# Kernel optimization log

Hardware: AMD Instinct MI355X
Metric: run time of the kernel (lower is better)

## Reference

```python
import jax, jax.numpy as jnp
import numpy as np

# --- static config (matches init_kwargs) ---
T, V, D, H = 4096, 32000, 1024, 16
DH = D // H                      # rope/head dim = 64
E, CAP, K, HOPS = 8, 1024, 2, 3  # non-identity experts, capacity, top-k, hops
MLP = 4 * D
ROPE_BASE = 10000.0
ATTN_IDX = np.array([0, 2, 4, 6])  # experts built with i%2==0 -> Attention
FFN_IDX = np.array([1, 3, 5, 7])   # i%2==1 -> FeedForward
EPS = 1e-6


def rope_cos_sin(t, dh, base):
    inv = 1.0 / (base ** (jnp.arange(0, dh, 2, dtype=jnp.float32) / dh))
    ang = jnp.arange(t, dtype=jnp.float32)[:, None] * inv[None, :]  # [T, dh/2]
    ang = jnp.concatenate([ang, ang], axis=-1)                      # [T, dh]
    return jnp.cos(ang), jnp.sin(ang)


def rotate_half(x):
    h = x.shape[-1] // 2
    return jnp.concatenate([-x[..., h:], x[..., :h]], axis=-1)


def topk_mask(logits, k):
    # boolean [T, E_total] mask of per-row top-k
    _, idx = jax.lax.top_k(logits, k)
    hard = jax.nn.one_hot(idx, logits.shape[-1]).sum(axis=-2)
    return hard.astype(bool)


def capacity_select(mask_te, gate_te, capacity):
    # mask_te: [T,E] bool, gate_te: [T,E] float -> slot [E,C,T], kept [E,T]
    m = mask_te.T                                   # [E, T]
    g = jnp.where(m, gate_te.T, -jnp.inf)           # [E, T]
    cap = int(min(capacity, g.shape[1]))
    _, top_idx = jax.lax.top_k(g, cap)              # [E, C]
    Ee, C = top_idx.shape
    slot = jnp.zeros((Ee, C, g.shape[1]), g.dtype)
    slot = slot.at[jnp.arange(Ee)[:, None], jnp.arange(C)[None, :], top_idx].set(1.0)
    slot = slot * m[:, None, :]                     # drop -inf fill slots
    kept = slot.sum(1).astype(bool)                 # [E, T]
    return slot, kept


def rms_norm(x, w):
    return x * jax.lax.rsqrt(jnp.mean(x * x, axis=-1, keepdims=True) + EPS) * w


def attention_group(x, cos_r, sin_r, wq, wk, wv, wo):
    # x: [G,C,D]; cos_r/sin_r: [G,C,DH]; weights: [G,D,D]
    G, C, _ = x.shape
    q = jnp.einsum('gcd,gde->gce', x, wq).reshape(G, C, H, DH)
    k = jnp.einsum('gcd,gde->gce', x, wk).reshape(G, C, H, DH)
    v = jnp.einsum('gcd,gde->gce', x, wv).reshape(G, C, H, DH)
    c = cos_r[:, :, None, :]
    s = sin_r[:, :, None, :]
    q = q * c + rotate_half(q) * s
    k = k * c + rotate_half(k) * s
    scores = jnp.einsum('gqhd,gkhd->ghqk', q, k) / np.sqrt(DH).astype(np.float32)
    attn = jax.nn.softmax(scores, axis=-1)
    out = jnp.einsum('ghqk,gkhd->gqhd', attn, v).reshape(G, C, D)
    return jnp.einsum('gcd,gde->gce', out, wo)


def ffn_group(x, w1, w2):
    # x: [G,C,D]; w1: [G,D,MLP]; w2: [G,MLP,D]
    return jnp.einsum('gcf,gfd->gcd', jax.nn.gelu(jnp.einsum('gcd,gdf->gcf', x, w1)), w2)


def dna_forward(ids, embed_w, router_w, wq, wk, wv, wo, w1, w2, ln_w):
    h = embed_w[ids]                                     # [T, D]
    cos, sin = rope_cos_sin(T, DH, ROPE_BASE)            # [T, DH]
    for hop in range(HOPS):
        logits = h @ router_w[hop].T                     # [T, E+1]
        probs = jax.nn.softmax(logits, axis=-1)
        mask_full = topk_mask(logits, K)                 # [T, E+1]
        probs_tr = probs[:, :-1]                         # [T, E]
        mask_tr = mask_full[:, :-1]
        slot, kept = capacity_select(mask_tr, probs_tr, CAP)  # [E,C,T], [E,T]
        # dispatch
        xin = jnp.einsum('ect,td->ecd', slot, h)          # [E, C, D]
        cos_r = jnp.einsum('ect,td->ecd', slot, cos)      # [E, C, DH]
        sin_r = jnp.einsum('ect,td->ecd', slot, sin)
        # grouped expert execution (stacked params, vectorized over group dim)
        attn_out = attention_group(xin[ATTN_IDX], cos_r[ATTN_IDX], sin_r[ATTN_IDX],
                                   wq, wk, wv, wo)        # [4, C, D]
        ffn_out = ffn_group(xin[FFN_IDX], w1, w2)         # [4, C, D]
        expert_out = jnp.zeros((E, CAP, D), h.dtype)
        expert_out = expert_out.at[ATTN_IDX].set(attn_out).at[FFN_IDX].set(ffn_out)
        # combine
        combine_w = jnp.where(kept.T, probs_tr, 0.0)      # [T, E]
        rho = combine_w.sum(axis=1, keepdims=True)        # [T, 1]
        combine = jnp.einsum('ecd,ect,et->td', expert_out, slot, combine_w.T)
        h = h + combine - rho * h
    return rms_norm(h, ln_w)


def setup_inputs() -> dict:
    key = jax.random.key(0)
    ks = jax.random.split(key, 10)
    sc = 0.02
    return {
        'ids': jax.random.randint(ks[0], (T,), 0, V),
        'embed_w': jax.random.normal(ks[1], (V, D), jnp.float32) * sc,
        'router_w': jax.random.normal(ks[2], (HOPS, E + 1, D), jnp.float32) * sc,
        'wq': jax.random.normal(ks[3], (4, D, D), jnp.float32) * sc,
        'wk': jax.random.normal(ks[4], (4, D, D), jnp.float32) * sc,
        'wv': jax.random.normal(ks[5], (4, D, D), jnp.float32) * sc,
        'wo': jax.random.normal(ks[6], (4, D, D), jnp.float32) * sc,
        'w1': jax.random.normal(ks[7], (4, D, MLP), jnp.float32) * sc,
        'w2': jax.random.normal(ks[8], (4, MLP, D), jnp.float32) * sc,
        'ln_w': jnp.ones((D,), jnp.float32),
    }


def reference(ids, embed_w, router_w, wq, wk, wv, wo, w1, w2, ln_w):
    return dna_forward(ids, embed_w, router_w, wq, wk, wv, wo, w1, w2, ln_w)
```

## Files before the change

kernel.cpp:

```cpp
#include <hip/hip_runtime.h>
#include <math.h>

#define T_ 4096
#define D_ 1024
#define H_ 16
#define DH_ 64
#define E_ 8
#define CAP_ 1024
#define MLP_ 4096
#define HOPS_ 3

__global__ __launch_bounds__(256) void embed_kernel(
    const int* __restrict__ ids, const float* __restrict__ ew, float* __restrict__ h)
{
  const int t = blockIdx.x;
  const int id = ids[t];
  const int c = threadIdx.x * 4;
  *(float4*)(h + (size_t)t * D_ + c) = *(const float4*)(ew + (size_t)id * D_ + c);
}

__global__ __launch_bounds__(64) void router_kernel(
    const float* __restrict__ h, const float* __restrict__ rw,
    float* __restrict__ probs, float* __restrict__ gmask)
{
  const int t = blockIdx.x;
  const int lane = threadIdx.x;
  __shared__ float hs[D_];
  #pragma unroll
  for (int j = 0; j < 4; ++j)
    *(float4*)&hs[lane * 4 + j * 256] = *(const float4*)(h + (size_t)t * D_ + lane * 4 + j * 256);
  __syncthreads();
  float l9[9];
  #pragma unroll
  for (int e = 0; e < 9; ++e) {
    float s = 0.0f;
    for (int i = lane; i < D_; i += 64) s += hs[i] * rw[e * D_ + i];
    #pragma unroll
    for (int off = 32; off > 0; off >>= 1) s += __shfl_down(s, off);
    l9[e] = s;
  }
  if (lane == 0) {
    float m = l9[0];
    #pragma unroll
    for (int e = 1; e < 9; ++e) m = fmaxf(m, l9[e]);
    float sum = 0.0f;
    float ex[9];
    #pragma unroll
    for (int e = 0; e < 9; ++e) { ex[e] = expf(l9[e] - m); sum += ex[e]; }
    const float inv = 1.0f / sum;
    int b1 = 0;
    #pragma unroll
    for (int e = 1; e < 9; ++e) if (l9[e] > l9[b1]) b1 = e;
    int b2 = (b1 == 0) ? 1 : 0;
    #pragma unroll
    for (int e = 0; e < 9; ++e) if (e != b1 && e != b2 && l9[e] > l9[b2]) b2 = e;
    #pragma unroll
    for (int e = 0; e < 8; ++e) {
      const float pe = ex[e] * inv;
      probs[t * 8 + e] = pe;
      gmask[(size_t)e * T_ + t] = (e == b1 || e == b2) ? pe : -1e30f;
    }
  }
}

__global__ __launch_bounds__(256) void zero_kernel(float* __restrict__ rho, int* __restrict__ cnt)
{
  const int i = blockIdx.x * 256 + threadIdx.x;
  if (i < T_) rho[i] = 0.0f;
  if (i < E_) cnt[i] = 0;
}

__global__ __launch_bounds__(256) void zeroeo_kernel(float* __restrict__ eo)
{
  const size_t i = ((size_t)blockIdx.x * 256 + threadIdx.x) * 4;
  float4 z; z.x = z.y = z.z = z.w = 0.0f;
  *(float4*)(eo + i) = z;
}

__global__ __launch_bounds__(256) void select_kernel(
    const float* __restrict__ gmask, const float* __restrict__ probs,
    int* __restrict__ idx, int* __restrict__ cnt, float* __restrict__ rho)
{
  __shared__ float row[T_];
  const int e = blockIdx.y;
  const int tid = threadIdx.x;
  const float* gr = gmask + (size_t)e * T_;
  #pragma unroll
  for (int j = 0; j < 16; ++j) row[tid + 256 * j] = gr[tid + 256 * j];
  __syncthreads();
  const int t = blockIdx.x * 256 + tid;
  const float g = row[t];
  if (g > -1e29f) {
    int rank = 0;
    for (int tt = 0; tt < T_; ++tt) {
      const float gg = row[tt];
      rank += (gg > g) || (gg == g && tt < t);
    }
    if (rank < CAP_) {
      const int pos = atomicAdd(&cnt[e], 1);
      idx[e * CAP_ + pos] = t;
      atomicAdd(&rho[t], probs[t * 8 + e]);
    }
  }
}

typedef __bf16 bf16x8 __attribute__((ext_vector_type(8)));
typedef float f32x4v __attribute__((ext_vector_type(4)));

union FragU { uint2 u2[2]; bf16x8 v; };

__device__ __forceinline__ unsigned pack_hi2(unsigned u0, unsigned u1)
{
  return (u0 >> 16) | (u1 & 0xFFFF0000u);
}

__device__ __forceinline__ void split8(const float4 a, const float4 b, FragU& h, FragU& l)
{
  const float f[8] = {a.x, a.y, a.z, a.w, b.x, b.y, b.z, b.w};
  unsigned hu[8], lu[8];
  #pragma unroll
  for (int i = 0; i < 8; ++i) {
    const unsigned u = __float_as_uint(f[i]);
    const float lo = f[i] - __uint_as_float(u & 0xFFFF0000u);
    hu[i] = u; lu[i] = __float_as_uint(lo);
  }
  h.u2[0].x = pack_hi2(hu[0], hu[1]); h.u2[0].y = pack_hi2(hu[2], hu[3]);
  h.u2[1].x = pack_hi2(hu[4], hu[5]); h.u2[1].y = pack_hi2(hu[6], hu[7]);
  l.u2[0].x = pack_hi2(lu[0], lu[1]); l.u2[0].y = pack_hi2(lu[2], lu[3]);
  l.u2[1].x = pack_hi2(lu[4], lu[5]); l.u2[1].y = pack_hi2(lu[6], lu[7]);
}

__device__ __forceinline__ void lds_load16(const void* g, void* l)
{
  __builtin_amdgcn_global_load_lds(
      (const __attribute__((address_space(1))) unsigned int*)g,
      (__attribute__((address_space(3))) unsigned int*)l, 16, 0, 0);
}

__device__ __forceinline__ float gelu_tanh(float x)
{
  const float x3 = x * x * x;
  return 0.5f * x * (1.0f + tanhf(0.7978845608028654f * (x + 0.044715f * x3)));
}

__global__ __launch_bounds__(256) void gather_kernel(
    const float* __restrict__ h, const int* __restrict__ idx, const int* __restrict__ cnt,
    unsigned short* __restrict__ xinp)
{
  const int c = blockIdx.x, e = blockIdx.y;
  const int c4 = threadIdx.x * 4;
  unsigned short* dst = xinp + ((size_t)e * CAP_ + c) * 2 * D_;
  if (c < cnt[e]) {
    const int t = idx[e * CAP_ + c];
    const float4 x = *(const float4*)(h + (size_t)t * D_ + c4);
    const float f[4] = {x.x, x.y, x.z, x.w};
    unsigned hu[4], lu[4];
    #pragma unroll
    for (int j = 0; j < 4; ++j) {
      const unsigned u = __float_as_uint(f[j]);
      const float lo = f[j] - __uint_as_float(u & 0xFFFF0000u);
      hu[j] = u; lu[j] = __float_as_uint(lo);
    }
    uint2 hp, lp;
    hp.x = pack_hi2(hu[0], hu[1]); hp.y = pack_hi2(hu[2], hu[3]);
    lp.x = pack_hi2(lu[0], lu[1]); lp.y = pack_hi2(lu[2], lu[3]);
    *(uint2*)(dst + c4) = hp;
    *(uint2*)(dst + D_ + c4) = lp;
  } else {
    uint2 z; z.x = 0u; z.y = 0u;
    *(uint2*)(dst + c4) = z;
    *(uint2*)(dst + D_ + c4) = z;
  }
}

__global__ __launch_bounds__(256) void convw_kernel(
    const float* __restrict__ W, unsigned short* __restrict__ out, int K, int N)
{
  const float* Wp = W + (size_t)blockIdx.z * K * N;
  unsigned short* op = out + (size_t)blockIdx.z * N * 2 * K;
  const int k0 = blockIdx.y * 64, n0 = blockIdx.x * 64;
  __shared__ float tile[64][65];
  const int tr = threadIdx.x >> 6;
  const int tc = threadIdx.x & 63;
  #pragma unroll
  for (int it = 0; it < 16; ++it) {
    const int r = it * 4 + tr;
    tile[r][tc] = Wp[(size_t)(k0 + r) * N + n0 + tc];
  }
  __syncthreads();
  #pragma unroll
  for (int it = 0; it < 16; ++it) {
    const int n = it * 4 + tr;
    const float f = tile[tc][n];
    const unsigned u = __float_as_uint(f);
    const float lo = f - __uint_as_float(u & 0xFFFF0000u);
    op[(size_t)(n0 + n) * 2 * K + k0 + tc] = (unsigned short)(u >> 16);
    op[(size_t)(n0 + n) * 2 * K + K + k0 + tc] = (unsigned short)(__float_as_uint(lo) >> 16);
  }
}

template <int EPI>
__device__ __forceinline__ void gemm_bf16_core(
    const unsigned short* __restrict__ A, const unsigned short* __restrict__ B,
    void* __restrict__ Cv, int N, int K, int vt0, int nvt)
{
  __shared__ unsigned short As[128 * 64];
  __shared__ unsigned short Bs[128 * 64];

  const int tid = threadIdx.x;
  const int lane = tid & 63;
  const int w = tid >> 6;
  const int wm = w >> 1, wn = w & 1;
  const int quad = lane >> 4, l15 = lane & 15;
  const int m0 = blockIdx.y * 128, n0 = blockIdx.x * 128;
  const size_t K2 = (size_t)2 * K;

  f32x4v acc[4][4];
  #pragma unroll
  for (int i = 0; i < 4; ++i)
    #pragma unroll
    for (int j = 0; j < 4; ++j) { acc[i][j][0] = 0.f; acc[i][j][1] = 0.f; acc[i][j][2] = 0.f; acc[i][j][3] = 0.f; }

  const int r0 = tid >> 3;
  const int c0 = (tid & 7) * 8;

  for (int vt = vt0; vt < vt0 + nvt; ++vt) {
    const int kk = vt / 3;
    const int ph = vt - kk * 3;
    const int ka = kk * 64 + (ph == 2 ? K : 0);
    const int kb = kk * 64 + (ph == 1 ? K : 0);
    __syncthreads();
    const unsigned short* Ag = A + (size_t)(m0 + r0) * K2 + ka + c0;
    const unsigned short* Bg = B + (size_t)(n0 + r0) * K2 + kb + c0;
    #pragma unroll
    for (int i = 0; i < 4; ++i)
      lds_load16(Ag + (size_t)(i * 32) * K2, &As[(tid + i * 256) * 8]);
    #pragma unroll
    for (int i = 0; i < 4; ++i)
      lds_load16(Bg + (size_t)(i * 32) * K2, &Bs[(tid + i * 256) * 8]);
    __syncthreads();
    #pragma unroll
    for (int ks = 0; ks < 2; ++ks) {
      FragU fa[4], fb[4];
      #pragma unroll
      for (int i = 0; i < 4; ++i) {
        const unsigned short* pa = &As[(wm * 64 + i * 16 + l15) * 64 + ks * 32 + quad * 8];
        fa[i].u2[0] = *(const uint2*)pa; fa[i].u2[1] = *(const uint2*)(pa + 4);
      }
      #pragma unroll
      for (int j = 0; j < 4; ++j) {
        const unsigned short* pb = &Bs[(wn * 64 + j * 16 + l15) * 64 + ks * 32 + quad * 8];
        fb[j].u2[0] = *(const uint2*)pb; fb[j].u2[1] = *(const uint2*)(pb + 4);
      }
      #pragma unroll
      for (int i = 0; i < 4; ++i)
        #pragma unroll
        for (int j = 0; j < 4; ++j)
          acc[i][j] = __builtin_amdgcn_mfma_f32_16x16x32_bf16(fa[i].v, fb[j].v, acc[i][j], 0, 0, 0);
    }
  }

  #pragma unroll
  for (int i = 0; i < 4; ++i)
    #pragma unroll
    for (int j = 0; j < 4; ++j) {
      const int n = n0 + wn * 64 + j * 16 + l15;
      #pragma unroll
      for (int r = 0; r < 4; ++r) {
        const int m = m0 + wm * 64 + i * 16 + quad * 4 + r;
        const float v = acc[i][j][r];
        if (EPI == 0) {
          ((float*)Cv)[(size_t)m * N + n] = v;
        } else if (EPI == 2) {
          atomicAdd(&((float*)Cv)[(size_t)m * N + n], v);
        } else {
          const float gv = gelu_tanh(v);
          const unsigned u = __float_as_uint(gv);
          const float lo = gv - __uint_as_float(u & 0xFFFF0000u);
          unsigned short* C = (unsigned short*)Cv;
          C[(size_t)m * 2 * N + n] = (unsigned short)(u >> 16);
          C[(size_t)m * 2 * N + N + n] = (unsigned short)(__float_as_uint(lo) >> 16);
        }
      }
    }
}

template <int EPI, int SK>
__global__ __launch_bounds__(256, 2) void gemm_bf16_k(
    const unsigned short* __restrict__ Ab, const unsigned short* __restrict__ Bb,
    void* __restrict__ Cb, int N, int K, long sA, long sB, long sC)
{
  const int z = blockIdx.z;
  const int g = z / SK, sp = z - g * SK;
  const unsigned short* A = Ab + (size_t)g * sA;
  const unsigned short* B = Bb + (size_t)g * sB;
  void* C;
  if (EPI == 1) C = (void*)((unsigned short*)Cb + (size_t)g * sC);
  else          C = (void*)((float*)Cb + (size_t)g * sC);
  const int kps = K / 64;
  const int per = 3 * kps / SK;
  gemm_bf16_core<EPI>(A, B, C, N, K, sp * per, per);
}

__global__ __launch_bounds__(256, 2) void gemm_qkv_bf16(
    const unsigned short* __restrict__ xinp,
    const unsigned short* __restrict__ wqp, const unsigned short* __restrict__ wkp,
    const unsigned short* __restrict__ wvp,
    float* __restrict__ qb, float* __restrict__ kb, float* __restrict__ vb)
{
  const int z = blockIdx.z;
  const int g = z & 3;
  const int which = z >> 2;
  const unsigned short* A = xinp + (size_t)(2 * g) * CAP_ * 2 * D_;
  const unsigned short* B = ((which == 0) ? wqp : (which == 1) ? wkp : wvp) + (size_t)g * D_ * 2 * D_;
  float* C = ((which == 0) ? qb : (which == 1) ? kb : vb) + (size_t)g * CAP_ * D_;
  gemm_bf16_core<0>(A, B, (void*)C, D_, D_, 0, 48);
}

__global__ __launch_bounds__(256) void rope_kernel(
    float* __restrict__ q, float* __restrict__ k,
    const int* __restrict__ idx, const int* __restrict__ cnt)
{
  const int c = blockIdx.x, g = blockIdx.y;
  const int e = 2 * g;
  if (c >= cnt[e]) return;
  const int t = idx[e * CAP_ + c];
  const int tid = threadIdx.x;
  const int hh = tid >> 4;
  const int pp = tid & 15;
  const size_t base = ((size_t)g * CAP_ + c) * D_ + hh * DH_;
  const float tf = (float)t;
  #pragma unroll
  for (int u = 0; u < 2; ++u) {
    const int i = pp * 2 + u;
    const float invf = (float)::pow(10000.0, -(double)i / 32.0);
    const float ang = tf * invf;
    const float cs = (float)::cos((double)ang);
    const float sn = (float)::sin((double)ang);
    const float q0 = q[base + i], q1 = q[base + i + 32];
    q[base + i]      = q0 * cs - q1 * sn;
    q[base + i + 32] = q1 * cs + q0 * sn;
    const float k0 = k[base + i], k1 = k[base + i + 32];
    k[base + i]      = k0 * cs - k1 * sn;
    k[base + i + 32] = k1 * cs + k0 * sn;
  }
}

#define FBQ 128
#define LDK 68
#define LDQ 72

__global__ __launch_bounds__(256, 2) void flash_mfma(
    const float* __restrict__ qg, const float* __restrict__ kg,
    const float* __restrict__ vg, unsigned short* __restrict__ og)
{
  const int g = blockIdx.z, hh = blockIdx.y, qt = blockIdx.x;
  const size_t base = (size_t)g * CAP_ * D_ + hh * DH_;
  const float* Q = qg + base;
  const float* Kp = kg + base;
  const float* Vp = vg + base;
  unsigned short* Ob = og + (size_t)g * CAP_ * 2 * D_ + hh * DH_;

  __shared__ __align__(16) char lds_raw[69632];
  unsigned short* Kh  = (unsigned short*)lds_raw;
  unsigned short* Kl  = Kh  + 64 * LDK;
  unsigned short* Vth = Kl  + 64 * LDK;
  unsigned short* Vtl = Vth + 64 * LDK;
  unsigned short* Ph  = Vtl + 64 * LDK;
  unsigned short* Pl  = Ph  + FBQ * LDK;
  float* Qs = (float*)lds_raw;

  const int tid = threadIdx.x;
  const int lane = tid & 63;
  const int w = tid >> 6;
  const int quad = lane >> 4;
  const int l15 = lane & 15;

  #pragma unroll
  for (int it = 0; it < 8; ++it) {
    const int row = it * 16 + (tid >> 4);
    const int c4 = (tid & 15) * 4;
    *(float4*)&Qs[row * LDQ + c4] = *(const float4*)(Q + (size_t)(qt * FBQ + row) * D_ + c4);
  }
  __syncthreads();
  FragU qf[2][2][2];
  #pragma unroll
  for (int rs = 0; rs < 2; ++rs)
    #pragma unroll
    for (int ks = 0; ks < 2; ++ks) {
      const float* p0 = &Qs[(w * 32 + rs * 16 + l15) * LDQ + ks * 32 + quad * 8];
      const float4 f0 = *(const float4*)p0;
      const float4 f1 = *(const float4*)(p0 + 4);
      split8(f0, f1, qf[rs][ks][0], qf[rs][ks][1]);
    }
  __syncthreads();

  f32x4v acc[2][4];
  float m_r[2][4], l_r[2][4];
  #pragma unroll
  for (int rs = 0; rs < 2; ++rs)
    #pragma unroll
    for (int r = 0; r < 4; ++r) { m_r[rs][r] = -1e30f; l_r[rs][r] = 0.0f; }
  #pragma unroll
  for (int rs = 0; rs < 2; ++rs)
    #pragma unroll
    for (int dt = 0; dt < 4; ++dt) { acc[rs][dt][0] = 0.f; acc[rs][dt][1] = 0.f; acc[rs][dt][2] = 0.f; acc[rs][dt][3] = 0.f; }

  for (int kt = 0; kt < 16; ++kt) {
    __syncthreads();
    #pragma unroll
    for (int it = 0; it < 4; ++it) {
      const int r = it * 16 + (tid >> 4);
      const int c4 = (tid & 15) * 4;
      const float4 kv = *(const float4*)(Kp + (size_t)(kt * 64 + r) * D_ + c4);
      {
        const unsigned u0 = __float_as_uint(kv.x), u1 = __float_as_uint(kv.y);
        const unsigned u2 = __float_as_uint(kv.z), u3 = __float_as_uint(kv.w);
        const float l0 = kv.x - __uint_as_float(u0 & 0xFFFF0000u);
        const float l1 = kv.y - __uint_as_float(u1 & 0xFFFF0000u);
        const float l2 = kv.z - __uint_as_float(u2 & 0xFFFF0000u);
        const float l3 = kv.w - __uint_as_float(u3 & 0xFFFF0000u);
        uint2 hp, lp;
        hp.x = pack_hi2(u0, u1); hp.y = pack_hi2(u2, u3);
        lp.x = pack_hi2(__float_as_uint(l0), __float_as_uint(l1));
        lp.y = pack_hi2(__float_as_uint(l2), __float_as_uint(l3));
        *(uint2*)&Kh[r * LDK + c4] = hp;
        *(uint2*)&Kl[r * LDK + c4] = lp;
      }
      const float4 vv = *(const float4*)(Vp + (size_t)(kt * 64 + r) * D_ + c4);
      const float vf[4] = {vv.x, vv.y, vv.z, vv.w};
      #pragma unroll
      for (int u = 0; u < 4; ++u) {
        const unsigned uu = __float_as_uint(vf[u]);
        const float lo = vf[u] - __uint_as_float(uu & 0xFFFF0000u);
        Vth[(c4 + u) * LDK + r] = (unsigned short)(uu >> 16);
        Vtl[(c4 + u) * LDK + r] = (unsigned short)(__float_as_uint(lo) >> 16);
      }
    }
    __syncthreads();
    f32x4v sfr[2][4];
    #pragma unroll
    for (int rs = 0; rs < 2; ++rs)
      #pragma unroll
      for (int j = 0; j < 4; ++j) {
        f32x4v s; s[0] = 0.f; s[1] = 0.f; s[2] = 0.f; s[3] = 0.f;
        #pragma unroll
        for (int ks = 0; ks < 2; ++ks) {
          FragU kh, kl;
          const unsigned short* pk = &Kh[(j * 16 + l15) * LDK + ks * 32 + quad * 8];
          const unsigned short* pl = &Kl[(j * 16 + l15) * LDK + ks * 32 + quad * 8];
          kh.u2[0] = *(const uint2*)pk; kh.u2[1] = *(const uint2*)(pk + 4);
          kl.u2[0] = *(const uint2*)pl; kl.u2[1] = *(const uint2*)(pl + 4);
          s = __builtin_amdgcn_mfma_f32_16x16x32_bf16(qf[rs][ks][0].v, kh.v, s, 0, 0, 0);
          s = __builtin_amdgcn_mfma_f32_16x16x32_bf16(qf[rs][ks][0].v, kl.v, s, 0, 0, 0);
          s = __builtin_amdgcn_mfma_f32_16x16x32_bf16(qf[rs][ks][1].v, kh.v, s, 0, 0, 0);
        }
        sfr[rs][j] = s;
      }
    #pragma unroll
    for (int rs = 0; rs < 2; ++rs) {
      #pragma unroll
      for (int r = 0; r < 4; ++r) {
        float s0 = sfr[rs][0][r] * 0.125f;
        float s1 = sfr[rs][1][r] * 0.125f;
        float s2 = sfr[rs][2][r] * 0.125f;
        float s3 = sfr[rs][3][r] * 0.125f;
        float mx = fmaxf(fmaxf(s0, s1), fmaxf(s2, s3));
        #pragma unroll
        for (int o = 1; o < 16; o <<= 1) mx = fmaxf(mx, __shfl_xor(mx, o));
        const float nm = fmaxf(m_r[rs][r], mx);
        const float al = __expf(m_r[rs][r] - nm);
        m_r[rs][r] = nm;
        const float p0 = __expf(s0 - nm);
        const float p1 = __expf(s1 - nm);
        const float p2 = __expf(s2 - nm);
        const float p3 = __expf(s3 - nm);
        float rsum = p0 + p1 + p2 + p3;
        #pragma unroll
        for (int o = 1; o < 16; o <<= 1) rsum += __shfl_xor(rsum, o);
        l_r[rs][r] = l_r[rs][r] * al + rsum;
        #pragma unroll
        for (int dt = 0; dt < 4; ++dt) acc[rs][dt][r] *= al;
        const int row = w * 32 + rs * 16 + quad * 4 + r;
        const float pv[4] = {p0, p1, p2, p3};
        #pragma unroll
        for (int j = 0; j < 4; ++j) {
          const unsigned u = __float_as_uint(pv[j]);
          const float lo = pv[j] - __uint_as_float(u & 0xFFFF0000u);
          Ph[row * LDK + j * 16 + l15] = (unsigned short)(u >> 16);
          Pl[row * LDK + j * 16 + l15] = (unsigned short)(__float_as_uint(lo) >> 16);
        }
      }
    }
    __syncthreads();
    FragU pf[2][2][2];
    #pragma unroll
    for (int rs = 0; rs < 2; ++rs)
      #pragma unroll
      for (int ks = 0; ks < 2; ++ks) {
        const unsigned short* ph = &Ph[(w * 32 + rs * 16 + l15) * LDK + ks * 32 + quad * 8];
        const unsigned short* pl = &Pl[(w * 32 + rs * 16 + l15) * LDK + ks * 32 + quad * 8];
        pf[rs][ks][0].u2[0] = *(const uint2*)ph; pf[rs][ks][0].u2[1] = *(const uint2*)(ph + 4);
        pf[rs][ks][1].u2[0] = *(const uint2*)pl; pf[rs][ks][1].u2[1] = *(const uint2*)(pl + 4);
      }
    #pragma unroll
    for (int dt = 0; dt < 4; ++dt)
      #pragma unroll
      for (int ks = 0; ks < 2; ++ks) {
        FragU vh, vl;
        const unsigned short* pv_ = &Vth[(dt * 16 + l15) * LDK + ks * 32 + quad * 8];
        const unsigned short* pl_ = &Vtl[(dt * 16 + l15) * LDK + ks * 32 + quad * 8];
        vh.u2[0] = *(const uint2*)pv_; vh.u2[1] = *(const uint2*)(pv_ + 4);
        vl.u2[0] = *(const uint2*)pl_; vl.u2[1] = *(const uint2*)(pl_ + 4);
        #pragma unroll
        for (int rs = 0; rs < 2; ++rs) {
          acc[rs][dt] = __builtin_amdgcn_mfma_f32_16x16x32_bf16(pf[rs][ks][0].v, vh.v, acc[rs][dt], 0, 0, 0);
          acc[rs][dt] = __builtin_amdgcn_mfma_f32_16x16x32_bf16(pf[rs][ks][0].v, vl.v, acc[rs][dt], 0, 0, 0);
          acc[rs][dt] = __builtin_amdgcn_mfma_f32_16x16x32_bf16(pf[rs][ks][1].v, vh.v, acc[rs][dt], 0, 0, 0);
        }
      }
  }
  #pragma unroll
  for (int rs = 0; rs < 2; ++rs)
    #pragma unroll
    for (int r = 0; r < 4; ++r) {
      const float inv = 1.0f / l_r[rs][r];
      const int row = qt * FBQ + w * 32 + rs * 16 + quad * 4 + r;
      #pragma unroll
      for (int dt = 0; dt < 4; ++dt) {
        const float v = acc[rs][dt][r] * inv;
        const unsigned u = __float_as_uint(v);
        const float lo = v - __uint_as_float(u & 0xFFFF0000u);
        Ob[(size_t)row * 2 * D_ + dt * 16 + l15] = (unsigned short)(u >> 16);
        Ob[(size_t)row * 2 * D_ + D_ + dt * 16 + l15] = (unsigned short)(__float_as_uint(lo) >> 16);
      }
    }
}

__global__ __launch_bounds__(256) void initnew_kernel(
    const float* __restrict__ h, const float* __restrict__ rho, float* __restrict__ hn)
{
  const int t = blockIdx.x;
  const float f = 1.0f - rho[t];
  const int c = threadIdx.x * 4;
  float4 x = *(const float4*)(h + (size_t)t * D_ + c);
  x.x *= f; x.y *= f; x.z *= f; x.w *= f;
  *(float4*)(hn + (size_t)t * D_ + c) = x;
}

__global__ __launch_bounds__(256) void scatter_kernel(
    const float* __restrict__ eo, const int* __restrict__ idx, const int* __restrict__ cnt,
    const float* __restrict__ probs, float* __restrict__ hn)
{
  const int c = blockIdx.x, e = blockIdx.y;
  if (c >= cnt[e]) return;
  const int t = idx[e * CAP_ + c];
  const float w = probs[t * 8 + e];
  const float* src = eo + ((size_t)e * CAP_ + c) * D_;
  float* dst = hn + (size_t)t * D_;
  const int c4 = threadIdx.x * 4;
  #pragma unroll
  for (int j = 0; j < 4; ++j) atomicAdd(dst + c4 + j, src[c4 + j] * w);
}

__global__ __launch_bounds__(256) void rms_kernel(
    const float* __restrict__ h, const float* __restrict__ w, float* __restrict__ out)
{
  const int t = blockIdx.x;
  const int c = threadIdx.x * 4;
  const float4 x = *(const float4*)(h + (size_t)t * D_ + c);
  float ss = x.x * x.x + x.y * x.y + x.z * x.z + x.w * x.w;
  #pragma unroll
  for (int off = 32; off > 0; off >>= 1) ss += __shfl_down(ss, off);
  __shared__ float wsum[4];
  __shared__ float sscale;
  const int lane = threadIdx.x & 63, wv = threadIdx.x >> 6;
  if (lane == 0) wsum[wv] = ss;
  __syncthreads();
  if (threadIdx.x == 0) {
    const float s = wsum[0] + wsum[1] + wsum[2] + wsum[3];
    sscale = 1.0f / sqrtf(s * (1.0f / (float)D_) + 1e-6f);
  }
  __syncthreads();
  const float sc = sscale;
  const float4 w4 = *(const float4*)(w + c);
  float4 o;
  o.x = x.x * sc * w4.x; o.y = x.y * sc * w4.y; o.z = x.z * sc * w4.z; o.w = x.w * sc * w4.w;
  *(float4*)(out + (size_t)t * D_ + c) = o;
}

extern "C" void kernel_launch(void* const* d_in, const int* in_sizes, int n_in,
                              void* d_out, int out_size, void* d_ws, size_t ws_size,
                              hipStream_t stream)
{
  (void)in_sizes; (void)n_in; (void)out_size; (void)ws_size;
  const int* ids = (const int*)d_in[0];
  const float* embed_w = (const float*)d_in[1];
  const float* router_w = (const float*)d_in[2];
  const float* wq = (const float*)d_in[3];
  const float* wk = (const float*)d_in[4];
  const float* wv = (const float*)d_in[5];
  const float* wo = (const float*)d_in[6];
  const float* w1 = (const float*)d_in[7];
  const float* w2 = (const float*)d_in[8];
  const float* lnw = (const float*)d_in[9];
  float* out = (float*)d_out;

  float* p = (float*)d_ws;
  const size_t TD = (size_t)T_ * D_;
  float* hA = p;    p += TD;
  float* hB = p;    p += TD;
  float* probs = p; p += (size_t)T_ * E_;
  float* gmask = p; p += (size_t)E_ * T_;
  float* rho = p;   p += T_;
  int* idx = (int*)p;   p += E_ * CAP_;
  int* cnt = (int*)p;   p += 16;
  float* eo = p;   p += (size_t)E_ * CAP_ * D_;
  float* qb = p;   p += (size_t)4 * CAP_ * D_;
  float* kb = p;   p += (size_t)4 * CAP_ * D_;
  float* vb = p;   p += (size_t)4 * CAP_ * D_;
  unsigned short* aob = (unsigned short*)p; p += (size_t)4 * CAP_ * D_;
  unsigned short* midp = (unsigned short*)qb;
  unsigned short* xinp = (unsigned short*)p; p += (size_t)E_ * CAP_ * D_;
  unsigned short* wqp = (unsigned short*)p; p += (size_t)4 * D_ * D_;
  unsigned short* wkp = (unsigned short*)p; p += (size_t)4 * D_ * D_;
  unsigned short* wvp = (unsigned short*)p; p += (size_t)4 * D_ * D_;
  unsigned short* wop = (unsigned short*)p; p += (size_t)4 * D_ * D_;
  unsigned short* w1p = (unsigned short*)p; p += (size_t)4 * D_ * MLP_;
  unsigned short* w2p = (unsigned short*)p; p += (size_t)4 * D_ * MLP_;

  convw_kernel<<<dim3(D_ / 64, D_ / 64, 4), 256, 0, stream>>>(wq, wqp, D_, D_);
  convw_kernel<<<dim3(D_ / 64, D_ / 64, 4), 256, 0, stream>>>(wk, wkp, D_, D_);
  convw_kernel<<<dim3(D_ / 64, D_ / 64, 4), 256, 0, stream>>>(wv, wvp, D_, D_);
  convw_kernel<<<dim3(D_ / 64, D_ / 64, 4), 256, 0, stream>>>(wo, wop, D_, D_);
  convw_kernel<<<dim3(MLP_ / 64, D_ / 64, 4), 256, 0, stream>>>(w1, w1p, D_, MLP_);
  convw_kernel<<<dim3(D_ / 64, MLP_ / 64, 4), 256, 0, stream>>>(w2, w2p, MLP_, D_);

  embed_kernel<<<T_, 256, 0, stream>>>(ids, embed_w, hA);
  float* cur = hA;
  float* nxt = hB;
  for (int hop = 0; hop < HOPS_; ++hop) {
    router_kernel<<<T_, 64, 0, stream>>>(cur, router_w + (size_t)hop * 9 * D_, probs, gmask);
    zero_kernel<<<16, 256, 0, stream>>>(rho, cnt);
    select_kernel<<<dim3(16, 8), 256, 0, stream>>>(gmask, probs, idx, cnt, rho);
    gather_kernel<<<dim3(CAP_, E_), 256, 0, stream>>>(cur, idx, cnt, xinp);
    gemm_qkv_bf16<<<dim3(D_ / 128, CAP_ / 128, 12), 256, 0, stream>>>(xinp, wqp, wkp, wvp, qb, kb, vb);
    rope_kernel<<<dim3(CAP_, 4), 256, 0, stream>>>(qb, kb, idx, cnt);
    flash_mfma<<<dim3(CAP_ / FBQ, 16, 4), 256, 0, stream>>>(qb, kb, vb, aob);
    zeroeo_kernel<<<8192, 256, 0, stream>>>(eo);
    gemm_bf16_k<2, 4><<<dim3(D_ / 128, CAP_ / 128, 16), 256, 0, stream>>>(
        aob, wop, (void*)eo, D_, D_,
        (long)CAP_ * 2 * D_, (long)D_ * 2 * D_, (long)2 * CAP_ * D_);
    gemm_bf16_k<1, 1><<<dim3(MLP_ / 128, CAP_ / 128, 4), 256, 0, stream>>>(
        xinp + (size_t)CAP_ * 2 * D_, w1p, (void*)midp, MLP_, D_,
        (long)2 * CAP_ * 2 * D_, (long)MLP_ * 2 * D_, (long)CAP_ * 2 * MLP_);
    gemm_bf16_k<2, 4><<<dim3(D_ / 128, CAP_ / 128, 16), 256, 0, stream>>>(
        midp, w2p, (void*)(eo + (size_t)CAP_ * D_), D_, MLP_,
        (long)CAP_ * 2 * MLP_, (long)D_ * 2 * MLP_, (long)2 * CAP_ * D_);
    initnew_kernel<<<T_, 256, 0, stream>>>(cur, rho, nxt);
    scatter_kernel<<<dim3(CAP_, E_), 256, 0, stream>>>(eo, idx, cnt, probs, nxt);
    float* tmp = cur; cur = nxt; nxt = tmp;
  }
  rms_kernel<<<T_, 256, 0, stream>>>(cur, lnw, out);
}
```

Measured before the change: 3.343 ms.

## Restructure split-bf16 GEMM tiles with XOR-swizzled LDS and XCD-aware block remap

Each LDS tile now holds both the hi and lo bf16 halves for a 32-wide k chunk, so one load round serves all three MFMA passes (hi*hi, hi*lo, lo*hi) and the A-hi fragments are reused across them. Earlier, each pass reloaded its own 64-wide tile. LDS columns are XOR-swizzled by row to avoid bank conflicts on fragment reads. Blocks are remapped so consecutive IDs spread across the 8 XCDs, aiming for better L2 locality. The cost is more fragment registers live at once and extra index arithmetic.

```diff
diff --git a/kernel.cpp b/kernel.cpp
--- a/kernel.cpp
+++ b/kernel.cpp
@@ -202,7 +202,7 @@
 template <int EPI>
 __device__ __forceinline__ void gemm_bf16_core(
     const unsigned short* __restrict__ A, const unsigned short* __restrict__ B,
-    void* __restrict__ Cv, int N, int K, int vt0, int nvt)
+    void* __restrict__ Cv, int N, int K, int kc0, int nkc, int m0, int n0)
 {
   __shared__ unsigned short As[128 * 64];
   __shared__ unsigned short Bs[128 * 64];
@@ -212,7 +212,6 @@
   const int w = tid >> 6;
   const int wm = w >> 1, wn = w & 1;
   const int quad = lane >> 4, l15 = lane & 15;
-  const int m0 = blockIdx.y * 128, n0 = blockIdx.x * 128;
   const size_t K2 = (size_t)2 * K;
 
   f32x4v acc[4][4];
@@ -222,42 +221,67 @@
     for (int j = 0; j < 4; ++j) { acc[i][j][0] = 0.f; acc[i][j][1] = 0.f; acc[i][j][2] = 0.f; acc[i][j][3] = 0.f; }
 
   const int r0 = tid >> 3;
-  const int c0 = (tid & 7) * 8;
-
-  for (int vt = vt0; vt < vt0 + nvt; ++vt) {
-    const int kk = vt / 3;
-    const int ph = vt - kk * 3;
-    const int ka = kk * 64 + (ph == 2 ? K : 0);
-    const int kb = kk * 64 + (ph == 1 ? K : 0);
+  const int pc = tid & 7;
+
+  for (int kc = kc0; kc < kc0 + nkc; ++kc) {
+    const int kb = kc * 32;
     __syncthreads();
-    const unsigned short* Ag = A + (size_t)(m0 + r0) * K2 + ka + c0;
-    const unsigned short* Bg = B + (size_t)(n0 + r0) * K2 + kb + c0;
+    #pragma unroll
+    for (int i = 0; i < 4; ++i) {
+      const int row = r0 + i * 32;
+      const int lc = pc ^ (row & 7);
+      const int goff = (lc < 4) ? (kb + lc * 8) : (K + kb + (lc - 4) * 8);
+      lds_load16(A + (size_t)(m0 + row) * K2 + goff, &As[(tid + i * 256) * 8]);
+    }
+    #pragma unroll
+    for (int i = 0; i < 4; ++i) {
+      const int row = r0 + i * 32;
+      const int lc = pc ^ (row & 7);
+      const int goff = (lc < 4) ? (kb + lc * 8) : (K + kb + (lc - 4) * 8);
+      lds_load16(B + (size_t)(n0 + row) * K2 + goff, &Bs[(tid + i * 256) * 8]);
+    }
+    __syncthreads();
+
+    FragU fah[4], fbh[4], fbl[4], fal[4];
+    #pragma unroll
+    for (int i = 0; i < 4; ++i) {
+      const int row = wm * 64 + i * 16 + l15;
+      const unsigned short* pr = &As[row * 64 + ((quad ^ (row & 7)) * 8)];
+      fah[i].u2[0] = *(const uint2*)pr; fah[i].u2[1] = *(const uint2*)(pr + 4);
+    }
+    #pragma unroll
+    for (int j = 0; j < 4; ++j) {
+      const int row = wn * 64 + j * 16 + l15;
+      const unsigned short* pr = &Bs[row * 64 + ((quad ^ (row & 7)) * 8)];
+      fbh[j].u2[0] = *(const uint2*)pr; fbh[j].u2[1] = *(const uint2*)(pr + 4);
+    }
     #pragma unroll
     for (int i = 0; i < 4; ++i)
-      lds_load16(Ag + (size_t)(i * 32) * K2, &As[(tid + i * 256) * 8]);
+      #pragma unroll
+      for (int j = 0; j < 4; ++j)
+        acc[i][j] = __builtin_amdgcn_mfma_f32_16x16x32_bf16(fah[i].v, fbh[j].v, acc[i][j], 0, 0, 0);
+    #pragma unroll
+    for (int j = 0; j < 4; ++j) {
+      const int row = wn * 64 + j * 16 + l15;
+      const unsigned short* pr = &Bs[row * 64 + (((quad + 4) ^ (row & 7)) * 8)];
+      fbl[j].u2[0] = *(const uint2*)pr; fbl[j].u2[1] = *(const uint2*)(pr + 4);
+    }
     #pragma unroll
     for (int i = 0; i < 4; ++i)
-      lds_load16(Bg + (size_t)(i * 32) * K2, &Bs[(tid + i * 256) * 8]);
-    __syncthreads();
-    #pragma unroll
-    for (int ks = 0; ks < 2; ++ks) {
-      FragU fa[4], fb[4];
-      #pragma unroll
-      for (int i = 0; i < 4; ++i) {
-        const unsigned short* pa = &As[(wm * 64 + i * 16 + l15) * 64 + ks * 32 + quad * 8];
-        fa[i].u2[0] = *(const uint2*)pa; fa[i].u2[1] = *(const uint2*)(pa + 4);
-      }
-      #pragma unroll
-      for (int j = 0; j < 4; ++j) {
-        const unsigned short* pb = &Bs[(wn * 64 + j * 16 + l15) * 64 + ks * 32 + quad * 8];
-        fb[j].u2[0] = *(const uint2*)pb; fb[j].u2[1] = *(const uint2*)(pb + 4);
-      }
-      #pragma unroll
-      for (int i = 0; i < 4; ++i)
-        #pragma unroll
-        for (int j = 0; j < 4; ++j)
-          acc[i][j] = __builtin_amdgcn_mfma_f32_16x16x32_bf16(fa[i].v, fb[j].v, acc[i][j], 0, 0, 0);
-    }
+      #pragma unroll
+      for (int j = 0; j < 4; ++j)
+        acc[i][j] = __builtin_amdgcn_mfma_f32_16x16x32_bf16(fah[i].v, fbl[j].v, acc[i][j], 0, 0, 0);
+    #pragma unroll
+    for (int i = 0; i < 4; ++i) {
+      const int row = wm * 64 + i * 16 + l15;
+      const unsigned short* pr = &As[row * 64 + (((quad + 4) ^ (row & 7)) * 8)];
+      fal[i].u2[0] = *(const uint2*)pr; fal[i].u2[1] = *(const uint2*)(pr + 4);
+    }
+    #pragma unroll
+    for (int i = 0; i < 4; ++i)
+      #pragma unroll
+      for (int j = 0; j < 4; ++j)
+        acc[i][j] = __builtin_amdgcn_mfma_f32_16x16x32_bf16(fal[i].v, fbh[j].v, acc[i][j], 0, 0, 0);
   }
 
   #pragma unroll
@@ -290,16 +314,22 @@
     const unsigned short* __restrict__ Ab, const unsigned short* __restrict__ Bb,
     void* __restrict__ Cb, int N, int K, long sA, long sB, long sC)
 {
-  const int z = blockIdx.z;
+  const int nx = gridDim.x, ny = gridDim.y;
+  const int total = nx * ny * gridDim.z;
+  int flat = blockIdx.x + nx * (blockIdx.y + ny * blockIdx.z);
+  int s = (flat & 7) * (total >> 3) + (flat >> 3);
+  const int bx = s % nx; s /= nx;
+  const int by = s % ny;
+  const int z = s / ny;
+
   const int g = z / SK, sp = z - g * SK;
   const unsigned short* A = Ab + (size_t)g * sA;
   const unsigned short* B = Bb + (size_t)g * sB;
   void* C;
   if (EPI == 1) C = (void*)((unsigned short*)Cb + (size_t)g * sC);
   else          C = (void*)((float*)Cb + (size_t)g * sC);
-  const int kps = K / 64;
-  const int per = 3 * kps / SK;
-  gemm_bf16_core<EPI>(A, B, C, N, K, sp * per, per);
+  const int nkc = (K / 32) / SK;
+  gemm_bf16_core<EPI>(A, B, C, N, K, sp * nkc, nkc, by * 128, bx * 128);
 }
 
 __global__ __launch_bounds__(256, 2) void gemm_qkv_bf16(
@@ -308,13 +338,20 @@
     const unsigned short* __restrict__ wvp,
     float* __restrict__ qb, float* __restrict__ kb, float* __restrict__ vb)
 {
-  const int z = blockIdx.z;
+  const int nx = gridDim.x, ny = gridDim.y;
+  const int total = nx * ny * gridDim.z;
+  int flat = blockIdx.x + nx * (blockIdx.y + ny * blockIdx.z);
+  int s = (flat & 7) * (total >> 3) + (flat >> 3);
+  const int bx = s % nx; s /= nx;
+  const int by = s % ny;
+  const int z = s / ny;
+
   const int g = z & 3;
   const int which = z >> 2;
   const unsigned short* A = xinp + (size_t)(2 * g) * CAP_ * 2 * D_;
   const unsigned short* B = ((which == 0) ? wqp : (which == 1) ? wkp : wvp) + (size_t)g * D_ * 2 * D_;
   float* C = ((which == 0) ? qb : (which == 1) ? kb : vb) + (size_t)g * CAP_ * D_;
-  gemm_bf16_core<0>(A, B, (void*)C, D_, D_, 0, 48);
+  gemm_bf16_core<0>(A, B, (void*)C, D_, D_, 0, 32, by * 128, bx * 128);
 }
 
 __global__ __launch_bounds__(256) void rope_kernel(
```

Result: faster. 2.724 ms (-18.5%).
